# Kernel tuning notes

Measured on AMD Instinct MI355X. Metric: run time of the kernel, lower is better.

Reference implementation:

```python
import jax, jax.numpy as jnp
import numpy as np

N = 25000      # nodes
E = 400000     # directed edges (avg degree 16)
F_IN = 133     # atom feature dim (QM_137k)
H = 8          # heads
C = 64         # hidden per head
HC = H * C     # 512
OUT = 1
NEG_SLOPE = 0.2
BN_EPS = 1e-5


def setup_inputs() -> dict:
    key = jax.random.key(0)
    ks = jax.random.split(key, 8)
    s = 0.05
    return {
        "x": jax.random.normal(ks[0], (N, F_IN), jnp.float32),
        "edge_index": jax.random.randint(ks[1], (2, E), 0, N, dtype=jnp.int32),
        # GATv2Conv params (share_weights=False): W_l for src, W_r for dst, att vector per head
        "Wl": jax.random.normal(ks[2], (F_IN, HC), jnp.float32) * s,
        "Wr": jax.random.normal(ks[3], (F_IN, HC), jnp.float32) * s,
        "att": jax.random.normal(ks[4], (H, C), jnp.float32) * s,
        "b1": jnp.zeros((HC,), jnp.float32),
        # BatchNorm1d (eval mode: running stats)
        "bn_gamma": jnp.ones((HC,), jnp.float32),
        "bn_beta": jnp.zeros((HC,), jnp.float32),
        "bn_mean": jnp.zeros((HC,), jnp.float32),
        "bn_var": jnp.ones((HC,), jnp.float32),
        # PReLU (default: single shared weight, init 0.25)
        "prelu_w": jnp.full((1,), 0.25, jnp.float32),
        # GCNConv params
        "Wg": jax.random.normal(ks[5], (HC, OUT), jnp.float32) * s,
        "bg": jnp.zeros((OUT,), jnp.float32),
    }


def _with_self_loops(edge_index):
    loops = jnp.arange(N, dtype=edge_index.dtype)
    src = jnp.concatenate([edge_index[0], loops])
    dst = jnp.concatenate([edge_index[1], loops])
    return src, dst


def _gatv2(x, edge_index, Wl, Wr, att, b1):
    # PyG GATv2Conv, concat=True, add_self_loops=True, eval (attention dropout off)
    src, dst = _with_self_loops(edge_index)
    xl = (x @ Wl).reshape(N, H, C)   # source-side transform
    xr = (x @ Wr).reshape(N, H, C)   # target-side transform
    msg = xl[src]                    # [E', H, C] gathered source messages
    e = jnp.einsum('ehc,hc->eh', jax.nn.leaky_relu(msg + xr[dst], NEG_SLOPE), att)  # [E', H]
    # segment softmax over incoming edges of each dst node (self loops => no empty segments)
    emax = jax.ops.segment_max(e, dst, num_segments=N)
    ee = jnp.exp(e - emax[dst])
    den = jax.ops.segment_sum(ee, dst, num_segments=N)
    agg = jax.ops.segment_sum(ee[:, :, None] * msg, dst, num_segments=N)  # [N, H, C]
    out = agg / den[:, :, None]
    return out.reshape(N, HC) + b1


def _gcn(x, edge_index, Wg, bg):
    # PyG GCNConv: add self loops, sym-normalized aggregation of x @ W, plus bias
    src, dst = _with_self_loops(edge_index)
    deg = jax.ops.segment_sum(jnp.ones_like(dst, dtype=x.dtype), dst, num_segments=N)
    dinv = jax.lax.rsqrt(jnp.maximum(deg, 1.0))
    h = x @ Wg                                   # [N, OUT]
    norm = dinv[src] * dinv[dst]                 # [E']
    return jax.ops.segment_sum(norm[:, None] * h[src], dst, num_segments=N) + bg


def reference(x, edge_index, Wl, Wr, att, b1, bn_gamma, bn_beta, bn_mean, bn_var,
              prelu_w, Wg, bg):
    h = _gatv2(x, edge_index, Wl, Wr, att, b1)
    # BatchNorm1d (eval) + PReLU
    h = (h - bn_mean) * jax.lax.rsqrt(bn_var + BN_EPS) * bn_gamma + bn_beta
    h = jnp.where(h >= 0, h, prelu_w * h)
    # dropout is identity in eval mode
    out = _gcn(h, edge_index, Wg, bg)
    return out.squeeze()  # [N]
```

## Files before the change

kernel.cpp:

```cpp
#include <hip/hip_runtime.h>

#define NN 25000
#define EE 400000
#define FIN 133
#define HCC 512
#define RPAD 25088
#define KPAD 160
#define NT 5
#define CAP 64
#define EPB 4082

typedef __attribute__((ext_vector_type(8))) __bf16 bf16x8;
typedef __attribute__((ext_vector_type(4))) float f32x4;
typedef __attribute__((ext_vector_type(8))) _Float16 f16x8;
typedef __attribute__((ext_vector_type(4))) _Float16 f16x4;
typedef __attribute__((ext_vector_type(2))) _Float16 f16x2;

static __device__ __forceinline__ ushort f2bf(float f) {
    uint32_t u = __float_as_uint(f);
    uint32_t r = (u + 0x7fffu + ((u >> 16) & 1u)) >> 16;
    return (ushort)r;
}
static __device__ __forceinline__ float bf2f(ushort b) {
    return __uint_as_float(((uint32_t)b) << 16);
}

static __device__ __forceinline__ f16x2 lrelu2(f16x2 t) {
#if __has_builtin(__builtin_elementwise_max) && __has_builtin(__builtin_elementwise_min)
    const f16x2 z = {(_Float16)0.f, (_Float16)0.f};
    const f16x2 c = {(_Float16)0.2f, (_Float16)0.2f};
    return __builtin_elementwise_min(t, z) * c + __builtin_elementwise_max(t, z);
#else
    f16x2 r;
    r[0] = t[0] >= (_Float16)0.f ? t[0] : (_Float16)((float)t[0] * 0.2f);
    r[1] = t[1] >= (_Float16)0.f ? t[1] : (_Float16)((float)t[1] * 0.2f);
    return r;
#endif
}
static __device__ __forceinline__ float fdot2f(f16x2 a, f16x2 b, float c) {
#if __has_builtin(__builtin_amdgcn_fdot2)
    return __builtin_amdgcn_fdot2(a, b, c, false);
#else
    return c + (float)a[0] * (float)b[0] + (float)a[1] * (float)b[1];
#endif
}

__global__ __launch_bounds__(256) void k_prep(const float* __restrict__ x,
    const float* __restrict__ Wl, const float* __restrict__ Wr,
    ushort* __restrict__ ah, ushort* __restrict__ al,
    ushort* __restrict__ wh, ushort* __restrict__ wl,
    const int* __restrict__ srcp, const int* __restrict__ dstp,
    int* __restrict__ cnt, int* __restrict__ csr,
    const float* __restrict__ att, const float* __restrict__ b1,
    const float* __restrict__ gam, const float* __restrict__ bet,
    const float* __restrict__ mean, const float* __restrict__ var,
    const float* __restrict__ Wg,
    float* __restrict__ attP, float* __restrict__ AP,
    float* __restrict__ BP, float* __restrict__ WgP)
{
    const int tid = threadIdx.x;
    const int y = blockIdx.y;
    if (y == 22) {
        if (blockIdx.x >= 2) return;
        int p = blockIdx.x * 256 + tid;
        int g = p >> 6, s = p & 63;
        int cl = s >> 2, j = s & 3;
        int c = (g << 6) | (j << 4) | cl;
        float sc = gam[c] * rsqrtf(var[c] + 1e-5f);
        attP[p] = att[c];
        AP[p] = sc;
        BP[p] = b1[c] * sc + (bet[c] - mean[c] * sc);
        WgP[p] = Wg[c];
        return;
    }
    if (y == 21) {
        int e0 = blockIdx.x * EPB;
        int e1 = e0 + EPB; if (e1 > EE) e1 = EE;
        for (int e = e0 + tid; e < e1; e += 256) {
            int d = dstp[e];
            int pos = atomicAdd(&cnt[d], 1);
            csr[d * CAP + pos] = srcp[e];
        }
        return;
    }
    if (y < 20) {
        const int row = blockIdx.x * 256 + tid;
        const int oct = y;
        const int kb = oct * 8;
        ushort h[8], l[8];
        #pragma unroll
        for (int j = 0; j < 8; ++j) {
            int k = kb + j;
            float v = (row < NN && k < FIN) ? x[(size_t)row * FIN + k] : 0.f;
            ushort hh = f2bf(v);
            h[j] = hh;
            l[j] = f2bf(v - bf2f(hh));
        }
        uint4 H, L;
        H.x = h[0] | (h[1] << 16); H.y = h[2] | (h[3] << 16);
        H.z = h[4] | (h[5] << 16); H.w = h[6] | (h[7] << 16);
        L.x = l[0] | (l[1] << 16); L.y = l[2] | (l[3] << 16);
        L.z = l[4] | (l[5] << 16); L.w = l[6] | (l[7] << 16);
        size_t slot = (size_t)oct * RPAD + row;
        ((uint4*)ah)[slot] = H;
        ((uint4*)al)[slot] = L;
    } else {
        if (blockIdx.x >= 80) return;
        const int oct = blockIdx.x >> 2;
        const int col = (blockIdx.x & 3) * 256 + tid;
        const int kb = oct * 8;
        const float* W = (col < 512) ? Wl : Wr;
        const int c = (col < 512) ? col : col - 512;
        ushort h[8], l[8];
        #pragma unroll
        for (int j = 0; j < 8; ++j) {
            int k = kb + j;
            float v = (k < FIN) ? W[(size_t)k * 512 + c] : 0.f;
            ushort hh = f2bf(v);
            h[j] = hh;
            l[j] = f2bf(v - bf2f(hh));
        }
        uint4 H, L;
        H.x = h[0] | (h[1] << 16); H.y = h[2] | (h[3] << 16);
        H.z = h[4] | (h[5] << 16); H.w = h[6] | (h[7] << 16);
        L.x = l[0] | (l[1] << 16); L.y = l[2] | (l[3] << 16);
        L.z = l[4] | (l[5] << 16); L.w = l[6] | (l[7] << 16);
        size_t slot = (size_t)oct * 1024 + col;
        ((uint4*)wh)[slot] = H;
        ((uint4*)wl)[slot] = L;
    }
}

__global__ __launch_bounds__(256) void k_gemm3(
    const ushort* __restrict__ ah, const ushort* __restrict__ al,
    const ushort* __restrict__ wh, const ushort* __restrict__ wl,
    ushort* __restrict__ xl, ushort* __restrict__ xr)
{
    const int tid = threadIdx.x;
    const int wid = tid >> 6, lane = tid & 63;
    const int row0 = blockIdx.y * 128;
    const int cb = blockIdx.x * 128;
    const bool isR = cb >= 512;
    const int oc0 = isR ? cb - 512 : cb;
    const int wr = wid >> 1, wc = wid & 1;
    const int kg = lane >> 4, r = lane & 15;

    const int arow = row0 + wr * 64 + r;
    const int bcol = cb + wc * 64 + r;

    f32x4 acc[4][4];
    #pragma unroll
    for (int i = 0; i < 4; ++i)
        #pragma unroll
        for (int j = 0; j < 4; ++j) acc[i][j] = (f32x4)0.f;

    bf16x8 cah[2][4], cal[2][4], cbh[2][4], cbl[2][4];
    #pragma unroll
    for (int i = 0; i < 4; ++i) {
        const size_t abase = (size_t)kg * RPAD + arow;
        const size_t bbase = (size_t)kg * 1024 + bcol;
        cah[0][i] = ((const bf16x8*)ah)[abase + i * 16];
        cal[0][i] = ((const bf16x8*)al)[abase + i * 16];
        cbh[0][i] = ((const bf16x8*)wh)[bbase + i * 16];
        cbl[0][i] = ((const bf16x8*)wl)[bbase + i * 16];
    }
    #pragma unroll
    for (int t = 0; t < NT; ++t) {
        const int cur = t & 1, nxt = cur ^ 1;
        if (t + 1 < NT) {
            const size_t abase = (size_t)((t + 1) * 4 + kg) * RPAD + arow;
            const size_t bbase = (size_t)((t + 1) * 4 + kg) * 1024 + bcol;
            #pragma unroll
            for (int i = 0; i < 4; ++i) {
                cah[nxt][i] = ((const bf16x8*)ah)[abase + i * 16];
                cal[nxt][i] = ((const bf16x8*)al)[abase + i * 16];
                cbh[nxt][i] = ((const bf16x8*)wh)[bbase + i * 16];
                cbl[nxt][i] = ((const bf16x8*)wl)[bbase + i * 16];
            }
        }
        #pragma unroll
        for (int i = 0; i < 4; ++i)
            #pragma unroll
            for (int j = 0; j < 4; ++j)
                acc[i][j] = __builtin_amdgcn_mfma_f32_16x16x32_bf16(cah[cur][i], cbh[cur][j], acc[i][j], 0, 0, 0);
        #pragma unroll
        for (int i = 0; i < 4; ++i)
            #pragma unroll
            for (int j = 0; j < 4; ++j)
                acc[i][j] = __builtin_amdgcn_mfma_f32_16x16x32_bf16(cah[cur][i], cbl[cur][j], acc[i][j], 0, 0, 0);
        #pragma unroll
        for (int i = 0; i < 4; ++i)
            #pragma unroll
            for (int j = 0; j < 4; ++j)
                acc[i][j] = __builtin_amdgcn_mfma_f32_16x16x32_bf16(cal[cur][i], cbh[cur][j], acc[i][j], 0, 0, 0);
    }
    ushort* __restrict__ outp = isR ? xr : xl;
    const int cl = lane & 15, rq = lane >> 4;
    const int scol = oc0 + wc * 64 + cl * 4;
    #pragma unroll
    for (int i = 0; i < 4; ++i) {
        #pragma unroll
        for (int rr = 0; rr < 4; ++rr) {
            int row = row0 + wr * 64 + i * 16 + rq * 4 + rr;
            if (row < NN) {
                f16x4 hv;
                #pragma unroll
                for (int j = 0; j < 4; ++j) hv[j] = (_Float16)acc[i][j][rr];
                *(f16x4*)&outp[(size_t)row * HCC + scol] = hv;
            }
        }
    }
}

__global__ __launch_bounds__(256) void k_gat(
    const ushort* __restrict__ xl, const ushort* __restrict__ xr,
    const float* __restrict__ attP, const float* __restrict__ AP,
    const float* __restrict__ BP, const float* __restrict__ WgP,
    const float* __restrict__ pw,
    const int* __restrict__ cnt, const int* __restrict__ csr,
    float* __restrict__ g, float* __restrict__ dinvp)
{
    const int lane = threadIdx.x & 63;
    const int node = blockIdx.x * 4 + (threadIdx.x >> 6);
    const int sb = lane * 8;
    f16x8 xv = *(const f16x8*)&xr[(size_t)node * HCC + sb];
    float4 a0 = *(const float4*)&attP[sb];
    float4 a1 = *(const float4*)&attP[sb + 4];
    f16x2 xrh[4], avh[4];
    {
        const f16x2* xp = (const f16x2*)&xv;
        xrh[0] = xp[0]; xrh[1] = xp[1]; xrh[2] = xp[2]; xrh[3] = xp[3];
    }
    avh[0] = {(_Float16)a0.x, (_Float16)a0.y};
    avh[1] = {(_Float16)a0.z, (_Float16)a0.w};
    avh[2] = {(_Float16)a1.x, (_Float16)a1.y};
    avh[3] = {(_Float16)a1.z, (_Float16)a1.w};
    float s = 0.f;
    float acc[8] = {0.f, 0.f, 0.f, 0.f, 0.f, 0.f, 0.f, 0.f};
    const int deg = cnt[node];
    const int beg = node * CAP;
    auto process = [&](f16x8 hv) {
        const f16x2* hp = (const f16x2*)&hv;
        float ep = 0.f;
        #pragma unroll
        for (int p = 0; p < 4; ++p) {
            f16x2 t = hp[p] + xrh[p];
            ep = fdot2f(lrelu2(t), avh[p], ep);
        }
        ep += __shfl_xor(ep, 1);
        ep += __shfl_xor(ep, 2);
        ep += __shfl_xor(ep, 4);
        float w = __expf(ep);
        s += w;
        const _Float16* he = (const _Float16*)&hv;
        #pragma unroll
        for (int k = 0; k < 8; ++k) acc[k] += w * (float)he[k];
    };
    auto row = [&](int srcn) -> f16x8 {
        return *(const f16x8*)&xl[(size_t)srcn * HCC + sb];
    };
    process(row(node));
    int j = 0;
    for (; j + 4 <= deg; j += 4) {
        int sA = csr[beg + j], sB = csr[beg + j + 1];
        int sC = csr[beg + j + 2], sD = csr[beg + j + 3];
        f16x8 hA = row(sA);
        f16x8 hB = row(sB);
        f16x8 hC = row(sC);
        f16x8 hD = row(sD);
        process(hA); process(hB); process(hC); process(hD);
    }
    for (; j < deg; ++j) process(row(csr[beg + j]));
    float inv = 1.f / s;
    float p_w = pw[0];
    float dot = 0.f;
    #pragma unroll
    for (int k = 0; k < 8; ++k) {
        int idx = sb + k;
        float v = (acc[k] * inv) * AP[idx] + BP[idx];
        v = v >= 0.f ? v : p_w * v;
        dot += v * WgP[idx];
    }
    dot += __shfl_xor(dot, 1);
    dot += __shfl_xor(dot, 2);
    dot += __shfl_xor(dot, 4);
    dot += __shfl_xor(dot, 8);
    dot += __shfl_xor(dot, 16);
    dot += __shfl_xor(dot, 32);
    if (lane == 0) {
        float dn = rsqrtf((float)(deg + 1));
        g[node] = dn * dot;
        dinvp[node] = dn;
    }
}

__global__ __launch_bounds__(256) void k_gcn(
    const float* __restrict__ g, const float* __restrict__ dinv,
    const int* __restrict__ cnt, const int* __restrict__ csr,
    const float* __restrict__ bg, float* __restrict__ out)
{
    int t = blockIdx.x * 256 + threadIdx.x;
    int node = t >> 2;
    int sub = t & 3;
    if (node >= NN) return;
    int deg = cnt[node];
    int base = node * CAP;
    float s = 0.f;
    for (int j = sub; j < deg; j += 4) s += g[csr[base + j]];
    s += __shfl_xor(s, 1);
    s += __shfl_xor(s, 2);
    if (sub == 0) out[node] = dinv[node] * (g[node] + s) + bg[0];
}

extern "C" void kernel_launch(void* const* d_in, const int* in_sizes, int n_in,
                              void* d_out, int out_size, void* d_ws, size_t ws_size,
                              hipStream_t stream)
{
    const float* x    = (const float*)d_in[0];
    const int*   ei   = (const int*)d_in[1];
    const float* Wl   = (const float*)d_in[2];
    const float* Wr   = (const float*)d_in[3];
    const float* att  = (const float*)d_in[4];
    const float* b1   = (const float*)d_in[5];
    const float* gam  = (const float*)d_in[6];
    const float* bet  = (const float*)d_in[7];
    const float* mean = (const float*)d_in[8];
    const float* var  = (const float*)d_in[9];
    const float* pw   = (const float*)d_in[10];
    const float* Wg   = (const float*)d_in[11];
    const float* bg   = (const float*)d_in[12];
    float* out = (float*)d_out;

    char* base = (char*)d_ws;
    size_t o = 0;
    ushort* xl  = (ushort*)(base + o); o += (size_t)NN * HCC * 2;
    ushort* xr  = (ushort*)(base + o); o += (size_t)NN * HCC * 2;
    o = (o + 15) & ~(size_t)15;
    float* g    = (float*)(base + o); o += NN * 4;
    float* dinv = (float*)(base + o); o += NN * 4;
    int*   cnt  = (int*)(base + o);   o += NN * 4;
    int*   csr  = (int*)(base + o);   o += (size_t)NN * CAP * 4;
    float* attP = (float*)(base + o); o += HCC * 4;
    float* AP   = (float*)(base + o); o += HCC * 4;
    float* BP   = (float*)(base + o); o += HCC * 4;
    float* WgP  = (float*)(base + o); o += HCC * 4;
    o = (o + 15) & ~(size_t)15;
    ushort* ah = (ushort*)(base + o); o += (size_t)RPAD * KPAD * 2;
    ushort* al = (ushort*)(base + o); o += (size_t)RPAD * KPAD * 2;
    ushort* wh = (ushort*)(base + o); o += (size_t)KPAD * 1024 * 2;
    ushort* wl = (ushort*)(base + o); o += (size_t)KPAD * 1024 * 2;

    const int* srcp = ei;
    const int* dstp = ei + EE;

    hipMemsetAsync(cnt, 0, NN * sizeof(int), stream);
    k_prep<<<dim3(98, 23), 256, 0, stream>>>(x, Wl, Wr, ah, al, wh, wl,
                                             srcp, dstp, cnt, csr,
                                             att, b1, gam, bet, mean, var, Wg,
                                             attP, AP, BP, WgP);
    k_gemm3<<<dim3(8, 196), 256, 0, stream>>>(ah, al, wh, wl, xl, xr);
    k_gat<<<NN / 4, 256, 0, stream>>>(xl, xr, attP, AP, BP, WgP, pw,
                                      cnt, csr, g, dinv);
    k_gcn<<<(NN * 4 + 255) / 256, 256, 0, stream>>>(g, dinv, cnt, csr, bg, out);
}
```

Measured before the change: 222.5 us.

## Coalesce prep conversion via LDS transpose and remap GEMM blocks for XCD locality

The prep kernel moves from a 2D grid with strided per-thread x reads to a flat grid. Its x and W conversion blocks read a contiguous tile, transpose it through shared memory, then write the packed bf16 hi/lo octets, so global reads become coalesced. The GEMM launch grid is padded to 200 rows and block ids are remapped so the blocks landing on one XCD share row tiles and reuse A in L2. The costs are extra LDS use in prep and some idle padded GEMM blocks.

```diff
diff --git a/kernel.cpp b/kernel.cpp
--- a/kernel.cpp
+++ b/kernel.cpp
@@ -9,6 +9,12 @@
 #define NT 5
 #define CAP 64
 #define EPB 4082
+
+#define PB_SCAT0 0
+#define PB_CVTX0 98
+#define PB_CVTW0 490
+#define PB_PERM0 506
+#define PB_TOTAL 508
 
 typedef __attribute__((ext_vector_type(8))) __bf16 bf16x8;
 typedef __attribute__((ext_vector_type(4))) float f32x4;
@@ -58,11 +64,70 @@
     float* __restrict__ attP, float* __restrict__ AP,
     float* __restrict__ BP, float* __restrict__ WgP)
 {
+    __shared__ __align__(16) ushort lh[20][64][8];
+    __shared__ __align__(16) ushort ll[20][64][8];
     const int tid = threadIdx.x;
-    const int y = blockIdx.y;
-    if (y == 22) {
-        if (blockIdx.x >= 2) return;
-        int p = blockIdx.x * 256 + tid;
+    const int bid = blockIdx.x;
+
+    if (bid < PB_CVTX0) {
+        int e0 = bid * EPB;
+        int e1 = e0 + EPB; if (e1 > EE) e1 = EE;
+        for (int e = e0 + tid; e < e1; e += 256) {
+            int d = dstp[e];
+            int pos = atomicAdd(&cnt[d], 1);
+            csr[d * CAP + pos] = srcp[e];
+        }
+        return;
+    }
+    if (bid < PB_CVTW0) {
+        const int r0 = (bid - PB_CVTX0) * 64;
+        for (int fi = tid; fi < 64 * FIN; fi += 256) {
+            int row = fi / FIN, k = fi - row * FIN;
+            int grow = r0 + row;
+            float v = (grow < NN) ? x[(size_t)r0 * FIN + fi] : 0.f;
+            ushort hh = f2bf(v);
+            lh[k >> 3][row][k & 7] = hh;
+            ll[k >> 3][row][k & 7] = f2bf(v - bf2f(hh));
+        }
+        for (int zi = tid; zi < 64 * (KPAD - FIN); zi += 256) {
+            int k = FIN + (zi >> 6), row = zi & 63;
+            lh[k >> 3][row][k & 7] = 0;
+            ll[k >> 3][row][k & 7] = 0;
+        }
+        __syncthreads();
+        for (int oi = tid; oi < 20 * 64; oi += 256) {
+            int oct = oi >> 6, row = oi & 63;
+            size_t slot = (size_t)oct * RPAD + r0 + row;
+            ((uint4*)ah)[slot] = *(const uint4*)&lh[oct][row][0];
+            ((uint4*)al)[slot] = *(const uint4*)&ll[oct][row][0];
+        }
+        return;
+    }
+    if (bid < PB_PERM0) {
+        const int c0 = (bid - PB_CVTW0) * 64;
+        for (int idx = tid; idx < KPAD * 64; idx += 256) {
+            int k = idx >> 6, c = idx & 63;
+            float v = 0.f;
+            if (k < FIN) {
+                int gcol = c0 + c;
+                v = (gcol < 512) ? Wl[(size_t)k * 512 + gcol]
+                                 : Wr[(size_t)k * 512 + gcol - 512];
+            }
+            ushort hh = f2bf(v);
+            lh[k >> 3][c][k & 7] = hh;
+            ll[k >> 3][c][k & 7] = f2bf(v - bf2f(hh));
+        }
+        __syncthreads();
+        for (int oi = tid; oi < 20 * 64; oi += 256) {
+            int oct = oi >> 6, c = oi & 63;
+            size_t slot = (size_t)oct * 1024 + c0 + c;
+            ((uint4*)wh)[slot] = *(const uint4*)&lh[oct][c][0];
+            ((uint4*)wl)[slot] = *(const uint4*)&ll[oct][c][0];
+        }
+        return;
+    }
+    {
+        int p = (bid - PB_PERM0) * 256 + tid;
         int g = p >> 6, s = p & 63;
         int cl = s >> 2, j = s & 3;
         int c = (g << 6) | (j << 4) | cl;
@@ -71,63 +136,6 @@
         AP[p] = sc;
         BP[p] = b1[c] * sc + (bet[c] - mean[c] * sc);
         WgP[p] = Wg[c];
-        return;
-    }
-    if (y == 21) {
-        int e0 = blockIdx.x * EPB;
-        int e1 = e0 + EPB; if (e1 > EE) e1 = EE;
-        for (int e = e0 + tid; e < e1; e += 256) {
-            int d = dstp[e];
-            int pos = atomicAdd(&cnt[d], 1);
-            csr[d * CAP + pos] = srcp[e];
-        }
-        return;
-    }
-    if (y < 20) {
-        const int row = blockIdx.x * 256 + tid;
-        const int oct = y;
-        const int kb = oct * 8;
-        ushort h[8], l[8];
-        #pragma unroll
-        for (int j = 0; j < 8; ++j) {
-            int k = kb + j;
-            float v = (row < NN && k < FIN) ? x[(size_t)row * FIN + k] : 0.f;
-            ushort hh = f2bf(v);
-            h[j] = hh;
-            l[j] = f2bf(v - bf2f(hh));
-        }
-        uint4 H, L;
-        H.x = h[0] | (h[1] << 16); H.y = h[2] | (h[3] << 16);
-        H.z = h[4] | (h[5] << 16); H.w = h[6] | (h[7] << 16);
-        L.x = l[0] | (l[1] << 16); L.y = l[2] | (l[3] << 16);
-        L.z = l[4] | (l[5] << 16); L.w = l[6] | (l[7] << 16);
-        size_t slot = (size_t)oct * RPAD + row;
-        ((uint4*)ah)[slot] = H;
-        ((uint4*)al)[slot] = L;
-    } else {
-        if (blockIdx.x >= 80) return;
-        const int oct = blockIdx.x >> 2;
-        const int col = (blockIdx.x & 3) * 256 + tid;
-        const int kb = oct * 8;
-        const float* W = (col < 512) ? Wl : Wr;
-        const int c = (col < 512) ? col : col - 512;
-        ushort h[8], l[8];
-        #pragma unroll
-        for (int j = 0; j < 8; ++j) {
-            int k = kb + j;
-            float v = (k < FIN) ? W[(size_t)k * 512 + c] : 0.f;
-            ushort hh = f2bf(v);
-            h[j] = hh;
-            l[j] = f2bf(v - bf2f(hh));
-        }
-        uint4 H, L;
-        H.x = h[0] | (h[1] << 16); H.y = h[2] | (h[3] << 16);
-        H.z = h[4] | (h[5] << 16); H.w = h[6] | (h[7] << 16);
-        L.x = l[0] | (l[1] << 16); L.y = l[2] | (l[3] << 16);
-        L.z = l[4] | (l[5] << 16); L.w = l[6] | (l[7] << 16);
-        size_t slot = (size_t)oct * 1024 + col;
-        ((uint4*)wh)[slot] = H;
-        ((uint4*)wl)[slot] = L;
     }
 }
 
@@ -136,10 +144,15 @@
     const ushort* __restrict__ wh, const ushort* __restrict__ wl,
     ushort* __restrict__ xl, ushort* __restrict__ xr)
 {
+    const int F = blockIdx.y * 8 + blockIdx.x;
+    const int xcd = F & 7, kq = F >> 3;
+    const int c = kq & 7, q = kq >> 3;
+    const int p = q * 8 + xcd;
+    if (p >= 196) return;
     const int tid = threadIdx.x;
     const int wid = tid >> 6, lane = tid & 63;
-    const int row0 = blockIdx.y * 128;
-    const int cb = blockIdx.x * 128;
+    const int row0 = p * 128;
+    const int cb = c * 128;
     const bool isR = cb >= 512;
     const int oc0 = isR ? cb - 512 : cb;
     const int wr = wid >> 1, wc = wid & 1;
@@ -354,11 +367,11 @@
     const int* dstp = ei + EE;
 
     hipMemsetAsync(cnt, 0, NN * sizeof(int), stream);
-    k_prep<<<dim3(98, 23), 256, 0, stream>>>(x, Wl, Wr, ah, al, wh, wl,
-                                             srcp, dstp, cnt, csr,
-                                             att, b1, gam, bet, mean, var, Wg,
-                                             attP, AP, BP, WgP);
-    k_gemm3<<<dim3(8, 196), 256, 0, stream>>>(ah, al, wh, wl, xl, xr);
+    k_prep<<<PB_TOTAL, 256, 0, stream>>>(x, Wl, Wr, ah, al, wh, wl,
+                                         srcp, dstp, cnt, csr,
+                                         att, b1, gam, bet, mean, var, Wg,
+                                         attP, AP, BP, WgP);
+    k_gemm3<<<dim3(8, 200), 256, 0, stream>>>(ah, al, wh, wl, xl, xr);
     k_gat<<<NN / 4, 256, 0, stream>>>(xl, xr, attP, AP, BP, WgP, pw,
                                       cnt, csr, g, dinv);
     k_gcn<<<(NN * 4 + 255) / 256, 256, 0, stream>>>(g, dinv, cnt, csr, bg, out);
```

After: 205.3 us. -7.7%, faster.
